# Kernel optimization log

Measured on AMD Instinct MI355X. Metric: run time of the kernel, lower is better.

## Reference

```python
import jax, jax.numpy as jnp
import numpy as np
from math import sqrt

B, S, D, H = 4, 2048, 1024, 16
DH = D // H          # 64
DF = 4 * D           # 4096
EPS = 1e-5
NEG = -1e9


def layer_norm(x, w, b):
    mu = jnp.mean(x, axis=-1, keepdims=True)
    var = jnp.mean((x - mu) ** 2, axis=-1, keepdims=True)
    return (x - mu) * jax.lax.rsqrt(var + EPS) * w + b


def setup_inputs() -> dict:
    key = jax.random.key(0)
    ks = jax.random.split(key, 16)
    s = 0.02
    return {
        "state": jax.random.normal(ks[0], (B, S, D), jnp.float32),
        "mask": jax.random.randint(ks[1], (B, S), 0, 2, jnp.int32),
        "ln1_w": jnp.ones((D,), jnp.float32),
        "ln1_b": jnp.zeros((D,), jnp.float32),
        "Wq": jax.random.normal(ks[2], (H, D, DH), jnp.float32) * s,
        "bq": jnp.zeros((H, DH), jnp.float32),
        "Wk": jax.random.normal(ks[3], (H, D, DH), jnp.float32) * s,
        "bk": jnp.zeros((H, DH), jnp.float32),
        "Wv": jax.random.normal(ks[4], (H, D, DH), jnp.float32) * s,
        "bv": jnp.zeros((H, DH), jnp.float32),
        "Wo": jax.random.normal(ks[5], (D, D), jnp.float32) * s,
        "bo": jnp.zeros((D,), jnp.float32),
        "ln2_w": jnp.ones((D,), jnp.float32),
        "ln2_b": jnp.zeros((D,), jnp.float32),
        "W1": jax.random.normal(ks[6], (D, DF), jnp.float32) * s,
        "b1": jnp.zeros((DF,), jnp.float32),
        "W2": jax.random.normal(ks[7], (DF, D), jnp.float32) * s,
        "b2": jnp.zeros((D,), jnp.float32),
    }


def reference(state, mask, ln1_w, ln1_b, Wq, bq, Wk, bk, Wv, bv, Wo, bo,
              ln2_w, ln2_b, W1, b1, W2, b2):
    # pre-norm attention block
    hidden = layer_norm(state, ln1_w, ln1_b)               # [B,S,D]
    q = jnp.einsum("bsd,hde->bhse", hidden, Wq) + bq[None, :, None, :]
    k = jnp.einsum("bsd,hde->bhse", hidden, Wk) + bk[None, :, None, :]
    v = jnp.einsum("bsd,hde->bhse", hidden, Wv) + bv[None, :, None, :]
    scores = jnp.einsum("bhse,bhte->bhst", q, k) / sqrt(DH)  # [B,H,S,S]
    scores = jnp.where(mask[:, None, None, :] == 0, NEG, scores)
    weights = jax.nn.softmax(scores, axis=-1)
    attended = jnp.einsum("bhst,bhte->bhse", weights, v)    # [B,H,S,DH]
    # concat heads in head order (matches torch cat over per-head outputs)
    attended = attended.transpose(0, 2, 1, 3).reshape(B, S, D)
    attn_out = attended @ Wo + bo
    output = state + attn_out
    # pre-norm FFN block (dropout=0 -> identity)
    hidden = layer_norm(output, ln2_w, ln2_b)
    ff = jax.nn.gelu(hidden @ W1 + b1, approximate=False) @ W2 + b2
    return output + ff
```

## Files before the change

### kernel.cpp

```cpp
#include <hip/hip_runtime.h>
#include <math.h>

#define B_  4
#define S_  2048
#define D_  1024
#define H_  16
#define DH_ 64
#define DF_ 4096
#define M_  8192

#define QSC 0.18033688011112042f

typedef __attribute__((ext_vector_type(8))) short bf8_t;
typedef __attribute__((ext_vector_type(4))) float f4_t;

#if defined(__has_builtin)
#if __has_builtin(__builtin_amdgcn_cvt_pk_bf16_f32)
#define HAVE_PKCVT 1
#endif
#if __has_builtin(__builtin_amdgcn_global_load_lds)
#define HAVE_ASYNC 1
#endif
#if __has_builtin(__builtin_amdgcn_exp2f)
#define EXP2F(x) __builtin_amdgcn_exp2f(x)
#else
#define EXP2F(x) __expf((x) * 0.69314718055994531f)
#endif
#else
#define EXP2F(x) __expf((x) * 0.69314718055994531f)
#endif

#define SBAR() __builtin_amdgcn_sched_barrier(0)

__device__ __forceinline__ unsigned pk_bf16(float lo, float hi) {
#ifdef HAVE_PKCVT
  auto r = __builtin_amdgcn_cvt_pk_bf16_f32(lo, hi);
  unsigned u; __builtin_memcpy(&u, &r, 4); return u;
#else
  union { float f; unsigned u; } a, b2; a.f = lo; b2.f = hi;
  unsigned ra = a.u + 0x7fffu + ((a.u >> 16) & 1u);
  unsigned rb = b2.u + 0x7fffu + ((b2.u >> 16) & 1u);
  return (ra >> 16) | (rb & 0xffff0000u);
#endif
}

__device__ __forceinline__ unsigned short f2bf(float x) {
  return (unsigned short)(pk_bf16(x, x) & 0xffffu);
}

__device__ __forceinline__ bf8_t upk8(unsigned u0, unsigned u1, unsigned u2, unsigned u3) {
  union { unsigned u[4]; bf8_t v; } c;
  c.u[0] = u0; c.u[1] = u1; c.u[2] = u2; c.u[3] = u3; return c.v;
}

__device__ __forceinline__ f4_t mfma32(bf8_t a, bf8_t b, f4_t c) {
  return __builtin_amdgcn_mfma_f32_16x16x32_bf16(a, b, c, 0, 0, 0);
}

__device__ __forceinline__ void async16(const void* g, void* l) {
#ifdef HAVE_ASYNC
  __builtin_amdgcn_global_load_lds((__attribute__((address_space(1))) void*)(g),
                                   (__attribute__((address_space(3))) void*)(l), 16, 0, 0);
#else
  *(uint4*)l = *(const uint4*)g;
#endif
}

__device__ __forceinline__ int sw(int row) { return row & 7; }


__global__ __launch_bounds__(256) void wtrans_kernel(const float* __restrict__ in,
                                                     unsigned short* __restrict__ out,
                                                     int K, int N) {
  const int k0 = blockIdx.x * 32, n0 = blockIdx.y * 32;
  __shared__ float t[32][33];
  const int tid = threadIdx.x;
#pragma unroll
  for (int i = 0; i < 4; i++) {
    int idx = i * 256 + tid; int r = idx >> 5, c = idx & 31;
    t[r][c] = in[(size_t)(k0 + r) * N + n0 + c];
  }
  __syncthreads();
#pragma unroll
  for (int i = 0; i < 4; i++) {
    int idx = i * 256 + tid; int r = idx >> 5, c = idx & 31;
    out[(size_t)(n0 + r) * K + k0 + c] = f2bf(t[c][r]);
  }
}

__global__ __launch_bounds__(256) void qkvpack_kernel(const float* __restrict__ Wq,
                                                      const float* __restrict__ Wk,
                                                      const float* __restrict__ Wv,
                                                      unsigned short* __restrict__ WqkvT) {
  const int z = blockIdx.z;
  const int sel = z >> 4, h = z & 15;
  const float* in = (sel == 0 ? Wq : sel == 1 ? Wk : Wv) + (size_t)h * D_ * DH_;
  const int k0 = blockIdx.x * 32, n0 = blockIdx.y * 32;
  __shared__ float t[32][33];
  const int tid = threadIdx.x;
#pragma unroll
  for (int i = 0; i < 4; i++) {
    int idx = i * 256 + tid; int r = idx >> 5, c = idx & 31;
    t[r][c] = in[(size_t)(k0 + r) * DH_ + n0 + c];
  }
  __syncthreads();
#pragma unroll
  for (int i = 0; i < 4; i++) {
    int idx = i * 256 + tid; int r = idx >> 5, c = idx & 31;
    int n = sel * 1024 + h * 64 + n0 + r;
    WqkvT[(size_t)n * D_ + k0 + c] = f2bf(t[c][r]);
  }
}

__global__ void biaspack_kernel(const float* __restrict__ bq, const float* __restrict__ bk,
                                const float* __restrict__ bv, float* __restrict__ bqkv) {
  int i = blockIdx.x * 256 + threadIdx.x;
  if (i < 3072) {
    int sel = i >> 10, j = i & 1023;
    const float* src = sel == 0 ? bq : sel == 1 ? bk : bv;
    bqkv[i] = src[j];
  }
}


__global__ __launch_bounds__(256) void ln_kernel(const float* __restrict__ x,
                                                 const float* __restrict__ w,
                                                 const float* __restrict__ bb,
                                                 unsigned short* __restrict__ out) {
  const int row = blockIdx.x;
  const float* xr = x + (size_t)row * D_;
  const int tid = threadIdx.x;
  float v[4]; float s = 0.f;
#pragma unroll
  for (int i = 0; i < 4; i++) { v[i] = xr[tid + i * 256]; s += v[i]; }
  __shared__ float red[8];
#pragma unroll
  for (int o = 32; o; o >>= 1) s += __shfl_xor(s, o, 64);
  const int wv = tid >> 6, ln = tid & 63;
  if (!ln) red[wv] = s;
  __syncthreads();
  float mean = (red[0] + red[1] + red[2] + red[3]) * (1.f / 1024.f);
  float s2 = 0.f;
#pragma unroll
  for (int i = 0; i < 4; i++) { float d = v[i] - mean; s2 += d * d; }
#pragma unroll
  for (int o = 32; o; o >>= 1) s2 += __shfl_xor(s2, o, 64);
  if (!ln) red[4 + wv] = s2;
  __syncthreads();
  float var = (red[4] + red[5] + red[6] + red[7]) * (1.f / 1024.f);
  float rstd = rsqrtf(var + 1e-5f);
#pragma unroll
  for (int i = 0; i < 4; i++) {
    int c = tid + i * 256;
    out[(size_t)row * D_ + c] = f2bf((v[i] - mean) * rstd * w[c] + bb[c]);
  }
}

__global__ __launch_bounds__(256) void ffn2red_kernel(float* __restrict__ out,
                                                      const float* __restrict__ P,
                                                      const float* __restrict__ resid,
                                                      const float* __restrict__ bias) {
  const size_t i = ((size_t)blockIdx.x * 256 + threadIdx.x) * 4;
  f4_t a  = *(const f4_t*)&out[i];
  f4_t p  = *(const f4_t*)&P[i];
  f4_t rr = *(const f4_t*)&resid[i];
  f4_t bb = *(const f4_t*)&bias[(int)(i & 1023)];
  *(f4_t*)&out[i] = a + p + rr + bb;
}

template <int EPI>
__global__ __launch_bounds__(256) void gemm_bt(const unsigned short* __restrict__ A,
                                               const unsigned short* __restrict__ Bt,
                                               const float* __restrict__ bias,
                                               const float* __restrict__ resid,
                                               unsigned short* __restrict__ outb,
                                               float* __restrict__ outf,
                                               int Ndim, int Kdim) {
  __shared__ __align__(16) unsigned short Asmem[4096];
  __shared__ __align__(16) unsigned short Bsmem[4096];
  const int tid = threadIdx.x;
  const int wave = tid >> 6, lane = tid & 63;
  const int quad = lane >> 4, l16 = lane & 15;
  const int wm = wave >> 1, wn = wave & 1;

  const int gx = gridDim.x;
  const int nwg = gx * (int)gridDim.y;
  const int lin = (int)blockIdx.y * gx + (int)blockIdx.x;
  const int swz = (lin & 7) * (nwg >> 3) + (lin >> 3);
  const int m0 = (swz / gx) * 128, n0 = (swz % gx) * 128;

  const f4_t fzero = {0.f, 0.f, 0.f, 0.f};
  f4_t acc[4][4];
#pragma unroll
  for (int i = 0; i < 4; i++)
#pragma unroll
    for (int j = 0; j < 4; j++) acc[i][j] = fzero;

  const int rowA = tid >> 2;
  const int kp = (tid & 3) * 8;

  for (int k0 = 0; k0 < Kdim; k0 += 32) {
    __syncthreads();
#pragma unroll
    for (int r = 0; r < 2; r++) {
      const int row = r * 64 + rowA;
      const int e = row * 32 + kp;
      async16(A  + (size_t)(m0 + row) * Kdim + k0 + kp, &Asmem[e]);
      async16(Bt + (size_t)(n0 + row) * Kdim + k0 + kp, &Bsmem[e]);
    }
    __syncthreads();

    bf8_t a[4], b[4];
#pragma unroll
    for (int i = 0; i < 4; i++) {
      a[i] = *(const bf8_t*)&Asmem[(wm * 64 + i * 16 + l16) * 32 + quad * 8];
      b[i] = *(const bf8_t*)&Bsmem[(wn * 64 + i * 16 + l16) * 32 + quad * 8];
    }
#pragma unroll
    for (int i = 0; i < 4; i++)
#pragma unroll
      for (int j = 0; j < 4; j++)
        acc[i][j] = mfma32(a[i], b[j], acc[i][j]);
  }

#pragma unroll
  for (int i = 0; i < 4; i++) {
#pragma unroll
    for (int j = 0; j < 4; j++) {
#pragma unroll
      for (int r = 0; r < 4; r++) {
        const int m = m0 + wm * 64 + i * 16 + quad * 4 + r;
        const int n = n0 + wn * 64 + j * 16 + l16;
        float v = acc[i][j][r] + bias[n];
        if constexpr (EPI == 2) v = 0.5f * v * (1.f + erff(v * 0.70710678118654752f));
        if constexpr (EPI == 1) {
          v += resid[(size_t)m * Ndim + n];
          outf[(size_t)m * Ndim + n] = v;
        } else {
          outb[(size_t)m * Ndim + n] = f2bf(v);
        }
      }
    }
  }
}

template <int EPI>
__global__ __launch_bounds__(512, 2) void gemm256(const unsigned short* __restrict__ A,
                                                  const unsigned short* __restrict__ Bt,
                                                  const float* __restrict__ bias,
                                                  const float* __restrict__ resid,
                                                  unsigned short* __restrict__ outb,
                                                  float* __restrict__ outf,
                                                  float* __restrict__ outf2,
                                                  unsigned short* __restrict__ vTout,
                                                  int Ndim, int Kdim, int Kstride) {
  __shared__ __align__(16) unsigned short Asm[32768];
  __shared__ __align__(16) unsigned short Bsm[32768];
  const int tid = threadIdx.x;
  const int wave = tid >> 6, lane = tid & 63;
  const int quad = lane >> 4, l16 = lane & 15;
  const int wm = wave >> 2, wn = wave & 3;

  const int gx = gridDim.x;
  const int nwg = gx * (int)gridDim.y;
  const int lin = (int)blockIdx.y * gx + (int)blockIdx.x;
  const int swz = (lin & 7) * (nwg >> 3) + (lin >> 3);
  const int m0 = (swz / gx) * 256, n0 = (swz % gx) * 256;
  const int kz = (int)blockIdx.z * Kdim;

  const int NT = Kdim >> 6;
  const int srow = lane >> 3, schk = lane & 7;

#define STAGE_A(t, row0) do {                                               \
    const int r_ = (row0) + srow;                                           \
    async16(A + (size_t)(m0 + r_) * Kstride + kz + (t) * 64 +               \
                ((schk ^ (r_ & 7)) << 3),                                   \
            &Asm[(((t) & 1) << 14) + ((row0) << 6)]); } while (0)
#define STAGE_B(t, row0) do {                                               \
    const int r_ = (row0) + srow;                                           \
    async16(Bt + (size_t)(n0 + r_) * Kstride + kz + (t) * 64 +              \
                 ((schk ^ (r_ & 7)) << 3),                                  \
            &Bsm[(((t) & 1) << 14) + ((row0) << 6)]); } while (0)
#define STAGE_FULL(t) do {                                                  \
    STAGE_A(t, wave * 8);       STAGE_A(t, 64 + wave * 8);                  \
    STAGE_A(t, 128 + wave * 8); STAGE_A(t, 192 + wave * 8);                 \
    STAGE_B(t, wave * 8);       STAGE_B(t, 64 + wave * 8);                  \
    STAGE_B(t, 128 + wave * 8); STAGE_B(t, 192 + wave * 8); } while (0)

#define AFR(bo, row, s) \
  (*(const bf8_t*)&Asm[(bo) + ((row) << 6) + ((((s) * 4 + quad) ^ ((row) & 7)) << 3)])
#define BFR(bo, row, s) \
  (*(const bf8_t*)&Bsm[(bo) + ((row) << 6) + ((((s) * 4 + quad) ^ ((row) & 7)) << 3)])

  const f4_t fzero = {0.f, 0.f, 0.f, 0.f};
  f4_t acc[8][4];
#pragma unroll
  for (int i = 0; i < 8; i++)
#pragma unroll
    for (int j = 0; j < 4; j++) acc[i][j] = fzero;

  STAGE_FULL(0);
  STAGE_FULL(1);
  asm volatile("s_waitcnt vmcnt(8)" ::: "memory");
  __builtin_amdgcn_s_barrier();
  SBAR();

  const int ar0 = wm << 7;
  const int br0 = wn << 6;

  for (int t = 0; t < NT; ++t) {
    const int bo = (t & 1) << 14;
    const bool pf = (t + 2) < NT;
    const int t2 = t + 2;
    bf8_t a0[8], b0[4], a1[8], b1[4];

#pragma unroll
    for (int i = 0; i < 8; i++) a0[i] = AFR(bo, ar0 + i * 16 + l16, 0);
#pragma unroll
    for (int j = 0; j < 4; j++) b0[j] = BFR(bo, br0 + j * 16 + l16, 0);
    SBAR();
#pragma unroll
    for (int i = 0; i < 8; i++) a1[i] = AFR(bo, ar0 + i * 16 + l16, 1);
#pragma unroll
    for (int j = 0; j < 4; j++) b1[j] = BFR(bo, br0 + j * 16 + l16, 1);
    asm volatile("s_waitcnt lgkmcnt(12)" ::: "memory");
    SBAR();

    __builtin_amdgcn_s_setprio(1);
#pragma unroll
    for (int i = 0; i < 8; i++)
#pragma unroll
      for (int j = 0; j < 4; j++)
        acc[i][j] = mfma32(a0[i], b0[j], acc[i][j]);
    __builtin_amdgcn_s_setprio(0);
    SBAR();

    asm volatile("s_waitcnt lgkmcnt(0)" ::: "memory");
    __builtin_amdgcn_s_barrier();

    if (pf) STAGE_FULL(t2);
    SBAR();

    __builtin_amdgcn_s_setprio(1);
#pragma unroll
    for (int i = 0; i < 8; i++)
#pragma unroll
      for (int j = 0; j < 4; j++)
        acc[i][j] = mfma32(a1[i], b1[j], acc[i][j]);
    __builtin_amdgcn_s_setprio(0);
    SBAR();

    if (pf) asm volatile("s_waitcnt vmcnt(8)" ::: "memory");
    else    asm volatile("s_waitcnt vmcnt(0)" ::: "memory");
    __builtin_amdgcn_s_barrier();
    SBAR();
  }

#undef STAGE_A
#undef STAGE_B
#undef STAGE_FULL
#undef AFR
#undef BFR

  if (EPI == 0 && n0 >= 2048) {
    const int bb2 = m0 >> 11;
    const int sb64 = (m0 & 2047) + (wm << 7);
#pragma unroll
    for (int mi = 0; mi < 8; mi++) {
      const int i4 = mi & 3;
      const int g0 = (i4 & 2) * 16 + 8 * quad + 4 * (i4 & 1);
      const int sbase = sb64 + (mi >> 2) * 64 + g0;
#pragma unroll
      for (int nj = 0; nj < 4; nj++) {
        const int n = n0 + wn * 64 + nj * 16 + l16;
        const int ef = n - 2048;
        const int hh = ef >> 6, e = ef & 63;
        const float bsv = bias[n];
        uint2 wq;
        wq.x = pk_bf16(acc[mi][nj][0] + bsv, acc[mi][nj][1] + bsv);
        wq.y = pk_bf16(acc[mi][nj][2] + bsv, acc[mi][nj][3] + bsv);
        *(uint2*)&vTout[(size_t)((bb2 * 16 + hh) * 64 + e) * S_ + sbase] = wq;
      }
    }
    return;
  }

  float* const pdst = (EPI == 3) ? (blockIdx.z ? outf2 : outf) : outf;
  const float sc = (EPI == 0 && n0 < 1024) ? QSC : 1.f;
#pragma unroll
  for (int mi = 0; mi < 8; mi++) {
#pragma unroll
    for (int nj = 0; nj < 4; nj++) {
      const int n = n0 + wn * 64 + nj * 16 + l16;
      const float bs = (EPI == 3) ? 0.f : bias[n];
#pragma unroll
      for (int r = 0; r < 4; r++) {
        const int m = m0 + wm * 128 + mi * 16 + quad * 4 + r;
        float v = acc[mi][nj][r] + bs;
        if constexpr (EPI == 0) v *= sc;
        if constexpr (EPI == 2) v = 0.5f * v * (1.f + erff(v * 0.70710678118654752f));
        if constexpr (EPI == 1) {
          v += resid[(size_t)m * Ndim + n];
          outf[(size_t)m * Ndim + n] = v;
        } else if constexpr (EPI == 3) {
          pdst[(size_t)m * Ndim + n] = v;
        } else {
          outb[(size_t)m * Ndim + n] = f2bf(v);
        }
      }
    }
  }
}


__global__ __launch_bounds__(256, 2) void attn_kernel(const unsigned short* __restrict__ qkv,
                                                      const unsigned short* __restrict__ vT,
                                                      const int* __restrict__ maskp,
                                                      unsigned short* __restrict__ attended) {
  const int tid = threadIdx.x, wv = tid >> 6, lane = tid & 63;
  const int quad = lane >> 4, l16 = lane & 15;

  const int lin = (int)blockIdx.y * (int)gridDim.x + (int)blockIdx.x;
  const int virt = (lin & 7) * 128 + (lin >> 3);
  const int q0 = (virt & 15) * 128;
  const int bh = virt >> 4, b = bh >> 4, h = bh & 15;

  __shared__ __align__(16) unsigned short KsmF[16384];
  __shared__ __align__(16) unsigned short VsmF[16384];
  __shared__ float biasf[2048];

  {
    const int4 mk0 = *(const int4*)&maskp[b * S_ + tid * 8];
    const int4 mk1 = *(const int4*)&maskp[b * S_ + tid * 8 + 4];
    f4_t bv0, bv1;
    bv0[0] = mk0.x ? 0.f : -8e9f; bv0[1] = mk0.y ? 0.f : -8e9f;
    bv0[2] = mk0.z ? 0.f : -8e9f; bv0[3] = mk0.w ? 0.f : -8e9f;
    bv1[0] = mk1.x ? 0.f : -8e9f; bv1[1] = mk1.y ? 0.f : -8e9f;
    bv1[2] = mk1.z ? 0.f : -8e9f; bv1[3] = mk1.w ? 0.f : -8e9f;
    *(f4_t*)&biasf[tid * 8] = bv0;
    *(f4_t*)&biasf[tid * 8 + 4] = bv1;
  }

#define STAGE_T(it, cb) do {                                                   \
    _Pragma("unroll")                                                          \
    for (int r_ = 0; r_ < 4; r_++) {                                           \
      const int cc = r_ * 256 + tid;                                           \
      const int krow = cc >> 3, kc = (cc & 7) ^ (krow & 7);                    \
      async16(qkv + (size_t)(b * S_ + (it) * 128 + krow) * 3072 + 1024 +       \
                  h * 64 + kc * 8,                                             \
              &KsmF[((cb) << 13) + cc * 8]);                                   \
      const int e_ = cc >> 4, hf = (cc >> 3) & 1, vc = (cc & 7) ^ (e_ & 7);    \
      async16(vT + (size_t)(bh * 64 + e_) * S_ + (it) * 128 + hf * 64 +        \
                  vc * 8,                                                      \
              &VsmF[((cb) << 13) + cc * 8]);                                   \
    } } while (0)

  bf8_t aq[2][2];
#pragma unroll
  for (int sb = 0; sb < 2; sb++) {
    const unsigned short* qrow =
        qkv + (size_t)(b * S_ + q0 + wv * 32 + sb * 16 + l16) * 3072 + h * 64;
    aq[sb][0] = *(const bf8_t*)(qrow + quad * 8);
    aq[sb][1] = *(const bf8_t*)(qrow + 32 + quad * 8);
  }

  const bf8_t ones8 = {0x3F80, 0x3F80, 0x3F80, 0x3F80, 0x3F80, 0x3F80, 0x3F80, 0x3F80};
  const f4_t fzero = {0.f, 0.f, 0.f, 0.f};
  f4_t o[2][4], lacc[2];
#pragma unroll
  for (int sb = 0; sb < 2; sb++) {
    lacc[sb] = fzero;
#pragma unroll
    for (int ee = 0; ee < 4; ee++) o[sb][ee] = fzero;
  }

  STAGE_T(0, 0);
  asm volatile("s_waitcnt lgkmcnt(0)" ::: "memory");
  __builtin_amdgcn_s_barrier();

  for (int it = 0; it < S_ / 128; ++it) {
    const int cb = it & 1;
    __builtin_amdgcn_s_barrier();
    if (it + 1 < S_ / 128) {
      STAGE_T(it + 1, cb ^ 1);
      asm volatile("s_waitcnt vmcnt(8)" ::: "memory");
    } else {
      asm volatile("s_waitcnt vmcnt(0)" ::: "memory");
    }
    __builtin_amdgcn_s_barrier();

#pragma unroll
    for (int th = 0; th < 2; th++) {
      f4_t sf[2][4];
#pragma unroll
      for (int jj = 0; jj < 4; jj++) {
        f4_t bi = *(const f4_t*)&biasf[it * 128 + th * 64 + jj * 16 + quad * 4];
        sf[0][jj] = bi;
        sf[1][jj] = bi;
      }
      __builtin_amdgcn_s_setprio(1);
#pragma unroll
      for (int jj = 0; jj < 4; jj++) {
        const int krow = th * 64 + jj * 16 + l16, sk = krow & 7;
        bf8_t kf0 = *(const bf8_t*)&KsmF[(cb << 13) + krow * 64 + ((quad ^ sk) << 3)];
        bf8_t kf1 = *(const bf8_t*)&KsmF[(cb << 13) + krow * 64 + (((quad + 4) ^ sk) << 3)];
        sf[0][jj] = mfma32(kf0, aq[0][0], sf[0][jj]);
        sf[0][jj] = mfma32(kf1, aq[0][1], sf[0][jj]);
        sf[1][jj] = mfma32(kf0, aq[1][0], sf[1][jj]);
        sf[1][jj] = mfma32(kf1, aq[1][1], sf[1][jj]);
      }
      __builtin_amdgcn_s_setprio(0);

      bf8_t pp[2][2];
#pragma unroll
      for (int sb = 0; sb < 2; sb++) {
#pragma unroll
        for (int h2 = 0; h2 < 2; h2++) {
          float p0 = EXP2F(sf[sb][2 * h2][0]),     p1 = EXP2F(sf[sb][2 * h2][1]);
          float p2 = EXP2F(sf[sb][2 * h2][2]),     p3 = EXP2F(sf[sb][2 * h2][3]);
          float p4 = EXP2F(sf[sb][2 * h2 + 1][0]), p5 = EXP2F(sf[sb][2 * h2 + 1][1]);
          float p6 = EXP2F(sf[sb][2 * h2 + 1][2]), p7 = EXP2F(sf[sb][2 * h2 + 1][3]);
          pp[sb][h2] = upk8(pk_bf16(p0, p1), pk_bf16(p2, p3),
                            pk_bf16(p4, p5), pk_bf16(p6, p7));
        }
        lacc[sb] = mfma32(ones8, pp[sb][0], lacc[sb]);
        lacc[sb] = mfma32(ones8, pp[sb][1], lacc[sb]);
      }

      __builtin_amdgcn_s_setprio(1);
#pragma unroll
      for (int ee = 0; ee < 4; ee++) {
        const int vrow = ee * 16 + l16, sv = vrow & 7;
#pragma unroll
        for (int h2 = 0; h2 < 2; h2++) {
          bf8_t vf = *(const bf8_t*)&VsmF[(cb << 13) + vrow * 128 +
                                          (((4 * h2 + quad) ^ sv) << 3)
                                          + th * 64];
          o[0][ee] = mfma32(vf, pp[0][h2], o[0][ee]);
          o[1][ee] = mfma32(vf, pp[1][h2], o[1][ee]);
        }
      }
      __builtin_amdgcn_s_setprio(0);
    }
  }

#undef STAGE_T

  float linv[2];
#pragma unroll
  for (int sb = 0; sb < 2; sb++) linv[sb] = 1.f / lacc[sb][0];

  __syncthreads();
#pragma unroll
  for (int sb = 0; sb < 2; sb++) {
    int srow = wv * 32 + sb * 16 + l16;
#pragma unroll
    for (int ee = 0; ee < 4; ee++) {
      unsigned w0 = pk_bf16(o[sb][ee][0] * linv[sb], o[sb][ee][1] * linv[sb]);
      unsigned w1 = pk_bf16(o[sb][ee][2] * linv[sb], o[sb][ee][3] * linv[sb]);
      uint2 wq; wq.x = w0; wq.y = w1;
      *(uint2*)&KsmF[srow * 72 + ee * 16 + quad * 4] = wq;
    }
  }
  __syncthreads();
#pragma unroll
  for (int it = 0; it < 4; it++) {
    int row = it * 32 + (tid >> 3), e0 = (tid & 7) * 8;
    bf8_t v = *(const bf8_t*)&KsmF[row * 72 + e0];
    *(bf8_t*)&attended[(size_t)(b * S_ + q0 + row) * D_ + h * 64 + e0] = v;
  }
}


extern "C" void kernel_launch(void* const* d_in, const int* in_sizes, int n_in,
                              void* d_out, int out_size, void* d_ws, size_t ws_size,
                              hipStream_t stream) {
  const float* state = (const float*)d_in[0];
  const int*   maskp = (const int*)d_in[1];
  const float* ln1w  = (const float*)d_in[2];
  const float* ln1b  = (const float*)d_in[3];
  const float* Wq    = (const float*)d_in[4];
  const float* bq    = (const float*)d_in[5];
  const float* Wk    = (const float*)d_in[6];
  const float* bk    = (const float*)d_in[7];
  const float* Wv    = (const float*)d_in[8];
  const float* bv    = (const float*)d_in[9];
  const float* Wo    = (const float*)d_in[10];
  const float* bo    = (const float*)d_in[11];
  const float* ln2w  = (const float*)d_in[12];
  const float* ln2b  = (const float*)d_in[13];
  const float* W1    = (const float*)d_in[14];
  const float* b1    = (const float*)d_in[15];
  const float* W2    = (const float*)d_in[16];
  const float* b2    = (const float*)d_in[17];

  char* w = (char*)d_ws;
  unsigned short* hidden = (unsigned short*)w; w += (size_t)M_ * D_ * 2;
  unsigned short* WqkvT  = (unsigned short*)w; w += (size_t)3072 * D_ * 2;
  unsigned short* WoT    = (unsigned short*)w; w += (size_t)D_ * D_ * 2;
  unsigned short* W1T    = (unsigned short*)w; w += (size_t)DF_ * D_ * 2;
  unsigned short* qkv    = (unsigned short*)w; w += (size_t)M_ * 3072 * 2;
  unsigned short* vT     = (unsigned short*)w; w += (size_t)M_ * D_ * 2;
  float*          outp   = (float*)w;          w += (size_t)M_ * D_ * 4;
  unsigned short* W2T    = (unsigned short*)w; w += (size_t)D_ * DF_ * 2;
  float*          bqkv   = (float*)w;          w += 3072 * 4;
  unsigned short* ff1    = qkv;
  float*          Pbuf   = (float*)hidden;

  qkvpack_kernel<<<dim3(32, 2, 48), 256, 0, stream>>>(Wq, Wk, Wv, WqkvT);
  wtrans_kernel<<<dim3(32, 32), 256, 0, stream>>>(Wo, WoT, D_, D_);
  wtrans_kernel<<<dim3(32, 128), 256, 0, stream>>>(W1, W1T, D_, DF_);
  wtrans_kernel<<<dim3(128, 32), 256, 0, stream>>>(W2, W2T, DF_, D_);
  biaspack_kernel<<<12, 256, 0, stream>>>(bq, bk, bv, bqkv);

  ln_kernel<<<M_, 256, 0, stream>>>(state, ln1w, ln1b, hidden);
  gemm256<0><<<dim3(3072 / 256, M_ / 256), 512, 0, stream>>>(
      hidden, WqkvT, bqkv, nullptr, qkv, nullptr, nullptr, vT, 3072, D_, D_);
  attn_kernel<<<dim3(S_ / 128, B_ * H_), 256, 0, stream>>>(qkv, vT, maskp, hidden);
  gemm_bt<1><<<dim3(D_ / 128, M_ / 128), 256, 0, stream>>>(hidden, WoT, bo, state,
                                                           nullptr, outp, D_, D_);
  ln_kernel<<<M_, 256, 0, stream>>>(outp, ln2w, ln2b, hidden);
  gemm256<2><<<dim3(DF_ / 256, M_ / 256), 512, 0, stream>>>(
      hidden, W1T, b1, nullptr, ff1, nullptr, nullptr, nullptr, DF_, D_, D_);
  gemm256<3><<<dim3(D_ / 256, M_ / 256, 2), 512, 0, stream>>>(
      ff1, W2T, nullptr, nullptr, nullptr, Pbuf, (float*)d_out, nullptr,
      D_, DF_ / 2, DF_);
  ffn2red_kernel<<<(M_ * D_) / 1024, 256, 0, stream>>>((float*)d_out, Pbuf, outp, b2);
}
```

Measured before the change: 537.7 us.

## Replace split-K FFN2 GEMM and reduction with dedicated fused 128x256 kernel

Drops the split-K FFN2 GEMM, which wrote two fp32 partial buffers, along with its separate reduction kernel. A new gemm_ffn2 kernel computes the full K=4096 reduction per 128x256 tile and applies the bias and residual add in its epilogue. This removes the partial-sum write and re-read traffic and one launch, in exchange for fewer, longer workgroups (256 tiles) with double-buffered async LDS staging. SBAR scheduling barriers are also sprinkled through the attention kernel to constrain instruction reordering.

```diff
diff --git a/kernel.cpp b/kernel.cpp
--- a/kernel.cpp
+++ b/kernel.cpp
@@ -154,18 +154,6 @@
     int c = tid + i * 256;
     out[(size_t)row * D_ + c] = f2bf((v[i] - mean) * rstd * w[c] + bb[c]);
   }
-}
-
-__global__ __launch_bounds__(256) void ffn2red_kernel(float* __restrict__ out,
-                                                      const float* __restrict__ P,
-                                                      const float* __restrict__ resid,
-                                                      const float* __restrict__ bias) {
-  const size_t i = ((size_t)blockIdx.x * 256 + threadIdx.x) * 4;
-  f4_t a  = *(const f4_t*)&out[i];
-  f4_t p  = *(const f4_t*)&P[i];
-  f4_t rr = *(const f4_t*)&resid[i];
-  f4_t bb = *(const f4_t*)&bias[(int)(i & 1023)];
-  *(f4_t*)&out[i] = a + p + rr + bb;
 }
 
 template <int EPI>
@@ -385,14 +373,13 @@
     return;
   }
 
-  float* const pdst = (EPI == 3) ? (blockIdx.z ? outf2 : outf) : outf;
   const float sc = (EPI == 0 && n0 < 1024) ? QSC : 1.f;
 #pragma unroll
   for (int mi = 0; mi < 8; mi++) {
 #pragma unroll
     for (int nj = 0; nj < 4; nj++) {
       const int n = n0 + wn * 64 + nj * 16 + l16;
-      const float bs = (EPI == 3) ? 0.f : bias[n];
+      const float bs = bias[n];
 #pragma unroll
       for (int r = 0; r < 4; r++) {
         const int m = m0 + wm * 128 + mi * 16 + quad * 4 + r;
@@ -402,11 +389,134 @@
         if constexpr (EPI == 1) {
           v += resid[(size_t)m * Ndim + n];
           outf[(size_t)m * Ndim + n] = v;
-        } else if constexpr (EPI == 3) {
-          pdst[(size_t)m * Ndim + n] = v;
         } else {
           outb[(size_t)m * Ndim + n] = f2bf(v);
         }
+      }
+    }
+  }
+  (void)outf2;
+}
+
+__global__ __launch_bounds__(512, 2) void gemm_ffn2(const unsigned short* __restrict__ A,
+                                                    const unsigned short* __restrict__ Bt,
+                                                    const float* __restrict__ bias,
+                                                    const float* __restrict__ resid,
+                                                    float* __restrict__ outf) {
+  __shared__ __align__(16) unsigned short Asm[16384];
+  __shared__ __align__(16) unsigned short Bsm[32768];
+  const int tid = threadIdx.x;
+  const int wave = tid >> 6, lane = tid & 63;
+  const int quad = lane >> 4, l16 = lane & 15;
+  const int wm = wave >> 2, wn = wave & 3;
+
+  const int gx = gridDim.x;
+  const int nwg = gx * (int)gridDim.y;
+  const int lin = (int)blockIdx.y * gx + (int)blockIdx.x;
+  const int swz = (lin & 7) * (nwg >> 3) + (lin >> 3);
+  const int m0 = (swz / gx) * 128, n0 = (swz % gx) * 256;
+
+  const int NT = DF_ >> 6;
+
+#define F2_STAGE(t) do {                                                     \
+    _Pragma("unroll")                                                        \
+    for (int r_ = 0; r_ < 2; r_++) {                                         \
+      const int ci = r_ * 512 + tid;                                         \
+      const int row = ci >> 3, c = (ci & 7) ^ (row & 7);                     \
+      async16(A + (size_t)(m0 + row) * DF_ + (t) * 64 + c * 8,               \
+              &Asm[(((t) & 1) << 13) + ci * 8]);                             \
+    }                                                                        \
+    _Pragma("unroll")                                                        \
+    for (int r_ = 0; r_ < 4; r_++) {                                         \
+      const int ci = r_ * 512 + tid;                                         \
+      const int row = ci >> 3, c = (ci & 7) ^ (row & 7);                     \
+      async16(Bt + (size_t)(n0 + row) * DF_ + (t) * 64 + c * 8,              \
+              &Bsm[(((t) & 1) << 14) + ci * 8]);                             \
+    } } while (0)
+
+#define F2_AFR(bo, row, s) \
+  (*(const bf8_t*)&Asm[(bo) + ((row) << 6) + ((((s) * 4 + quad) ^ ((row) & 7)) << 3)])
+#define F2_BFR(bo, row, s) \
+  (*(const bf8_t*)&Bsm[(bo) + ((row) << 6) + ((((s) * 4 + quad) ^ ((row) & 7)) << 3)])
+
+  const f4_t fzero = {0.f, 0.f, 0.f, 0.f};
+  f4_t acc[4][4];
+#pragma unroll
+  for (int i = 0; i < 4; i++)
+#pragma unroll
+    for (int j = 0; j < 4; j++) acc[i][j] = fzero;
+
+  F2_STAGE(0);
+  F2_STAGE(1);
+  asm volatile("s_waitcnt vmcnt(6)" ::: "memory");
+  __builtin_amdgcn_s_barrier();
+  SBAR();
+
+  const int ar0 = wm << 6;
+  const int br0 = wn << 6;
+
+  for (int t = 0; t < NT; ++t) {
+    const int boA = (t & 1) << 13, boB = (t & 1) << 14;
+    const bool pf = (t + 2) < NT;
+    const int t2 = t + 2;
+    bf8_t a0[4], b0[4], a1[4], b1[4];
+
+#pragma unroll
+    for (int i = 0; i < 4; i++) a0[i] = F2_AFR(boA, ar0 + i * 16 + l16, 0);
+#pragma unroll
+    for (int j = 0; j < 4; j++) b0[j] = F2_BFR(boB, br0 + j * 16 + l16, 0);
+    SBAR();
+#pragma unroll
+    for (int i = 0; i < 4; i++) a1[i] = F2_AFR(boA, ar0 + i * 16 + l16, 1);
+#pragma unroll
+    for (int j = 0; j < 4; j++) b1[j] = F2_BFR(boB, br0 + j * 16 + l16, 1);
+    asm volatile("s_waitcnt lgkmcnt(8)" ::: "memory");
+    SBAR();
+
+    __builtin_amdgcn_s_setprio(1);
+#pragma unroll
+    for (int i = 0; i < 4; i++)
+#pragma unroll
+      for (int j = 0; j < 4; j++)
+        acc[i][j] = mfma32(a0[i], b0[j], acc[i][j]);
+    __builtin_amdgcn_s_setprio(0);
+    SBAR();
+
+    asm volatile("s_waitcnt lgkmcnt(0)" ::: "memory");
+    __builtin_amdgcn_s_barrier();
+
+    if (pf) F2_STAGE(t2);
+    SBAR();
+
+    __builtin_amdgcn_s_setprio(1);
+#pragma unroll
+    for (int i = 0; i < 4; i++)
+#pragma unroll
+      for (int j = 0; j < 4; j++)
+        acc[i][j] = mfma32(a1[i], b1[j], acc[i][j]);
+    __builtin_amdgcn_s_setprio(0);
+    SBAR();
+
+    if (pf) asm volatile("s_waitcnt vmcnt(6)" ::: "memory");
+    else    asm volatile("s_waitcnt vmcnt(0)" ::: "memory");
+    __builtin_amdgcn_s_barrier();
+    SBAR();
+  }
+
+#undef F2_STAGE
+#undef F2_AFR
+#undef F2_BFR
+
+#pragma unroll
+  for (int i = 0; i < 4; i++) {
+#pragma unroll
+    for (int j = 0; j < 4; j++) {
+      const int n = n0 + wn * 64 + j * 16 + l16;
+      const float bs = bias[n];
+#pragma unroll
+      for (int r = 0; r < 4; r++) {
+        const int m = m0 + wm * 64 + i * 16 + quad * 4 + r;
+        outf[(size_t)m * D_ + n] = acc[i][j][r] + bs + resid[(size_t)m * D_ + n];
       }
     }
   }
@@ -477,17 +587,21 @@
   STAGE_T(0, 0);
   asm volatile("s_waitcnt lgkmcnt(0)" ::: "memory");
   __builtin_amdgcn_s_barrier();
+  SBAR();
 
   for (int it = 0; it < S_ / 128; ++it) {
     const int cb = it & 1;
     __builtin_amdgcn_s_barrier();
+    SBAR();
     if (it + 1 < S_ / 128) {
       STAGE_T(it + 1, cb ^ 1);
+      SBAR();
       asm volatile("s_waitcnt vmcnt(8)" ::: "memory");
     } else {
       asm volatile("s_waitcnt vmcnt(0)" ::: "memory");
     }
     __builtin_amdgcn_s_barrier();
+    SBAR();
 
 #pragma unroll
     for (int th = 0; th < 2; th++) {
@@ -510,6 +624,7 @@
         sf[1][jj] = mfma32(kf1, aq[1][1], sf[1][jj]);
       }
       __builtin_amdgcn_s_setprio(0);
+      SBAR();
 
       bf8_t pp[2][2];
 #pragma unroll
@@ -526,6 +641,7 @@
         lacc[sb] = mfma32(ones8, pp[sb][0], lacc[sb]);
         lacc[sb] = mfma32(ones8, pp[sb][1], lacc[sb]);
       }
+      SBAR();
 
       __builtin_amdgcn_s_setprio(1);
 #pragma unroll
@@ -541,6 +657,7 @@
         }
       }
       __builtin_amdgcn_s_setprio(0);
+      SBAR();
     }
   }
 
@@ -605,7 +722,6 @@
   unsigned short* W2T    = (unsigned short*)w; w += (size_t)D_ * DF_ * 2;
   float*          bqkv   = (float*)w;          w += 3072 * 4;
   unsigned short* ff1    = qkv;
-  float*          Pbuf   = (float*)hidden;
 
   qkvpack_kernel<<<dim3(32, 2, 48), 256, 0, stream>>>(Wq, Wk, Wv, WqkvT);
   wtrans_kernel<<<dim3(32, 32), 256, 0, stream>>>(Wo, WoT, D_, D_);
@@ -622,8 +738,6 @@
   ln_kernel<<<M_, 256, 0, stream>>>(outp, ln2w, ln2b, hidden);
   gemm256<2><<<dim3(DF_ / 256, M_ / 256), 512, 0, stream>>>(
       hidden, W1T, b1, nullptr, ff1, nullptr, nullptr, nullptr, DF_, D_, D_);
-  gemm256<3><<<dim3(D_ / 256, M_ / 256, 2), 512, 0, stream>>>(
-      ff1, W2T, nullptr, nullptr, nullptr, Pbuf, (float*)d_out, nullptr,
-      D_, DF_ / 2, DF_);
-  ffn2red_kernel<<<(M_ * D_) / 1024, 256, 0, stream>>>((float*)d_out, Pbuf, outp, b2);
-}
+  gemm_ffn2<<<dim3(D_ / 256, M_ / 128), 512, 0, stream>>>(
+      ff1, W2T, b2, outp, (float*)d_out);
+}
```

Measured after the change: 621.4 us. 1.16x slower.
